# Performance work log

Hardware: AMD Instinct MI355X
Metric: run time of the kernel (lower is better)

## Reference

```python
import jax, jax.numpy as jnp
import numpy as np

NUM_EMBEDDINGS = 16384
EMBED_DIM = 256
COMMITMENT_COST = 0.25  # legacy=True: vq_loss = commit + beta * codebook


def setup_inputs() -> dict:
    key = jax.random.key(0)
    k1, k2, k3, k4 = jax.random.split(key, 4)
    z = jax.random.normal(k1, (8, 2048, EMBED_DIM), dtype=jnp.float32)
    # frozen codebook: normal(0, embedding_dim ** -0.5)
    codebook = jax.random.normal(k2, (NUM_EMBEDDINGS, EMBED_DIM), dtype=jnp.float32) * (EMBED_DIM ** -0.5)
    # learnable linear projection, torch default uniform init
    bound = 1.0 / np.sqrt(EMBED_DIM)
    proj_w = jax.random.uniform(k3, (EMBED_DIM, EMBED_DIM), dtype=jnp.float32, minval=-bound, maxval=bound)
    proj_b = jax.random.uniform(k4, (EMBED_DIM,), dtype=jnp.float32, minval=-bound, maxval=bound)
    return {"z": z, "codebook": codebook, "proj_w": proj_w, "proj_b": proj_b}


def reference(z, codebook, proj_w, proj_b):
    B, T, D = z.shape
    # projected codebook (the only learned part of the quantizer)
    quant_codebook = codebook @ proj_w.T + proj_b  # [K, D]
    z_flat = z.reshape(-1, D)  # [N, D]
    # squared L2 distances: ||z||^2 + ||c||^2 - 2 z.c
    dists = (
        jnp.sum(z_flat * z_flat, axis=1, keepdims=True)
        + jnp.sum(quant_codebook * quant_codebook, axis=1)
        - 2.0 * jnp.einsum("nd,kd->nk", z_flat, quant_codebook)
    )  # [N, K]
    idx = jnp.argmin(dists, axis=1)  # [N]
    quantized = quant_codebook[idx].reshape(z.shape)  # [B, T, D]

    commitment_loss = jnp.mean((jax.lax.stop_gradient(quantized) - z) ** 2)
    codebook_loss = jnp.mean((quantized - jax.lax.stop_gradient(z)) ** 2)
    vq_loss = commitment_loss + COMMITMENT_COST * codebook_loss  # legacy formulation

    # straight-through estimator
    quantized = z + jax.lax.stop_gradient(quantized - z)
    encoding_indices = idx.reshape(B, T)
    return quantized, vq_loss, encoding_indices
```

## Files before the change

### kernel.cpp

```cpp
#include <hip/hip_runtime.h>

typedef unsigned short u16;
typedef __bf16 bf16x8 __attribute__((ext_vector_type(8)));
typedef float f32x4 __attribute__((ext_vector_type(4)));

#define NQ 16384
#define NC 16384
#define DD 256
#define BM 256
#define BN 256
#define BK 32
#define NSPLIT 8
#define NPART (NSPLIT * 2)
#define NTILES ((NC / NSPLIT) / BN)
#define NSTEPS (NTILES * 8)

__device__ __forceinline__ u16 f2bf(float x) {
  unsigned u = __float_as_uint(x);
  u += 0x7fffu + ((u >> 16) & 1u);
  return (u16)(u >> 16);
}
__device__ __forceinline__ float bf2f(u16 h) {
  return __uint_as_float(((unsigned)h) << 16);
}

__device__ __forceinline__ void gl2lds16(const void* g, void* l) {
  __builtin_amdgcn_global_load_lds((__attribute__((address_space(1))) void*)g,
                                   (__attribute__((address_space(3))) void*)l,
                                   16, 0, 0);
}

#define MFMA_AGPR(ACC, A, B) \
  asm("v_mfma_f32_16x16x32_bf16 %0, %1, %2, %0" : "+a"(ACC) : "v"(A), "v"(B))

__global__ __launch_bounds__(256) void split_z_kernel(const float* __restrict__ z,
                                                      u16* __restrict__ Ah,
                                                      u16* __restrict__ Al) {
  size_t i = (size_t)blockIdx.x * 256 + threadIdx.x;
  float4 v = ((const float4*)z)[i];
  float f[4] = {v.x, v.y, v.z, v.w};
  u16 hh[4], ll[4];
#pragma unroll
  for (int j = 0; j < 4; ++j) {
    hh[j] = f2bf(f[j]);
    ll[j] = f2bf(f[j] - bf2f(hh[j]));
  }
  ushort4 h; h.x = hh[0]; h.y = hh[1]; h.z = hh[2]; h.w = hh[3];
  ushort4 l; l.x = ll[0]; l.y = ll[1]; l.z = ll[2]; l.w = ll[3];
  ((ushort4*)Ah)[i] = h;
  ((ushort4*)Al)[i] = l;
}

__global__ __launch_bounds__(256) void norm256_kernel(const float* __restrict__ x,
                                                      float* __restrict__ nrm) {
  const int t = threadIdx.x;
  const int j = t & 7;
  const int row = blockIdx.x * 32 + (t >> 3);
  const float* q = x + (size_t)row * 256;
  float half[2];
#pragma unroll
  for (int h = 0; h < 2; ++h) {
    const float* p = q + h * 128;
    float v0 = p[j];
    float r = __fmul_rn(v0, v0);
#pragma unroll
    for (int i = 8; i < 128; i += 8) {
      float v = p[i + j];
      r = __fadd_rn(r, __fmul_rn(v, v));
    }
    float s1 = __fadd_rn(r, __shfl_xor(r, 1));
    float s2 = __fadd_rn(s1, __shfl_xor(s1, 2));
    half[h] = __fadd_rn(s2, __shfl_xor(s2, 4));
  }
  if (j == 0) nrm[row] = __fadd_rn(half[0], half[1]);
}

__global__ __launch_bounds__(256) void qc_gemm_kernel(const float* __restrict__ cb,
                                                      const float* __restrict__ W,
                                                      const float* __restrict__ bias,
                                                      float* __restrict__ qc) {
  __shared__ float As[64][33];
  __shared__ float Bs[64][33];
  const int bm = blockIdx.x >> 2;
  const int bn = blockIdx.x & 3;
  const int m0 = bm * 64, n0 = bn * 64;
  const int t = threadIdx.x;
  const int tx = t & 15, ty = t >> 4;
  float acc[4][4] = {};
  for (int kc = 0; kc < 256; kc += 32) {
    __syncthreads();
#pragma unroll
    for (int j = 0; j < 8; ++j) {
      int idx = j * 256 + t;
      int r = idx >> 5, c = idx & 31;
      As[r][c] = cb[(size_t)(m0 + r) * 256 + kc + c];
      Bs[r][c] = W[(size_t)(n0 + r) * 256 + kc + c];
    }
    __syncthreads();
#pragma unroll
    for (int kk = 0; kk < 32; ++kk) {
      float a[4], b[4];
#pragma unroll
      for (int u = 0; u < 4; ++u) a[u] = As[ty * 4 + u][kk];
#pragma unroll
      for (int v = 0; v < 4; ++v) b[v] = Bs[tx * 4 + v][kk];
#pragma unroll
      for (int u = 0; u < 4; ++u)
#pragma unroll
        for (int v = 0; v < 4; ++v) acc[u][v] += a[u] * b[v];
    }
  }
#pragma unroll
  for (int u = 0; u < 4; ++u)
#pragma unroll
    for (int v = 0; v < 4; ++v) {
      int r = m0 + ty * 4 + u, c = n0 + tx * 4 + v;
      qc[(size_t)r * 256 + c] = acc[u][v] + bias[c];
    }
}

__global__ __launch_bounds__(256) void split_qc_kernel(const float* __restrict__ qc,
                                                       u16* __restrict__ Bh,
                                                       u16* __restrict__ Bl) {
  size_t i = (size_t)blockIdx.x * 256 + threadIdx.x;
  float4 v = ((const float4*)qc)[i];
  float f[4] = {v.x, v.y, v.z, v.w};
  u16 hh[4], ll[4];
#pragma unroll
  for (int j = 0; j < 4; ++j) {
    hh[j] = f2bf(f[j]);
    ll[j] = f2bf(f[j] - bf2f(hh[j]));
  }
  ushort4 h; h.x = hh[0]; h.y = hh[1]; h.z = hh[2]; h.w = hh[3];
  ushort4 l; l.x = ll[0]; l.y = ll[1]; l.z = ll[2]; l.w = ll[3];
  ((ushort4*)Bh)[i] = h;
  ((ushort4*)Bl)[i] = l;
}

__global__ __launch_bounds__(512, 2) void vq_argmin_kernel(
    const u16* __restrict__ Ah, const u16* __restrict__ Al,
    const u16* __restrict__ Bh, const u16* __restrict__ Bl,
    const float* __restrict__ cnorm, const float* __restrict__ znorm,
    float* __restrict__ pval, int* __restrict__ pidx) {
  __shared__ __align__(16) u16 Ahs[2][BM * BK];
  __shared__ __align__(16) u16 Als[2][BM * BK];
  __shared__ __align__(16) u16 Bhs[2][BN * BK];
  __shared__ __align__(16) u16 Bls[2][BN * BK];

  const int bm = blockIdx.x / NSPLIT;
  const int spl = blockIdx.x % NSPLIT;
  const int lane = threadIdx.x & 63;
  const int wid = threadIdx.x >> 6;
  const int wm = wid >> 1, wn = wid & 1;
  const int l15 = lane & 15;
  const int lg = lane >> 4;
  const int m0 = bm * BM;
  const int ns0 = spl * (NC / NSPLIT);

  const int st_r = lane >> 2;
  const int st_k = (((lane & 3) ^ ((lane >> 3) & 3)) << 3);

  const int rd_sw = ((lg ^ ((l15 >> 1) & 3)) << 3);

  auto stage = [&](int buf, int s) {
    const int ntt = s >> 3;
    const int kcc = (s & 7) * BK;
    const int nn0 = ns0 + ntt * BN;
#pragma unroll
    for (int j = 0; j < 2; ++j) {
      const int grp = wid * 2 + j;
      const int r = grp * 16 + st_r;
      const size_t ga = (size_t)(m0 + r) * DD + kcc + st_k;
      const size_t gb = (size_t)(nn0 + r) * DD + kcc + st_k;
      gl2lds16(Ah + ga, &Ahs[buf][grp * 512]);
      gl2lds16(Al + ga, &Als[buf][grp * 512]);
      gl2lds16(Bh + gb, &Bhs[buf][grp * 512]);
      gl2lds16(Bl + gb, &Bls[buf][grp * 512]);
    }
  };

  float rmin[4][4];
  int ridx[4][4];
#pragma unroll
  for (int a = 0; a < 4; ++a)
#pragma unroll
    for (int b = 0; b < 4; ++b) { rmin[a][b] = 3.4e38f; ridx[a][b] = 0; }

  stage(0, 0);
  asm volatile("s_waitcnt vmcnt(0)" ::: "memory");
  __builtin_amdgcn_s_barrier();

  for (int nt = 0; nt < NTILES; ++nt) {
    const int n0 = ns0 + nt * BN;
    f32x4 acc[4][8];
#pragma unroll
    for (int a = 0; a < 4; ++a)
#pragma unroll
      for (int b = 0; b < 8; ++b) {
        f32x4 zz = {0.f, 0.f, 0.f, 0.f};
        acc[a][b] = zz;
      }

#pragma unroll 1
    for (int k8 = 0; k8 < 8; ++k8) {
      const int s = nt * 8 + k8;
      const int cur = s & 1;

      __builtin_amdgcn_s_barrier();
      if (s + 1 < NSTEPS) {
        stage(cur ^ 1, s + 1);
        asm volatile("s_waitcnt vmcnt(8)" ::: "memory");
      } else {
        asm volatile("s_waitcnt vmcnt(0)" ::: "memory");
      }
      __builtin_amdgcn_s_barrier();
      __builtin_amdgcn_sched_barrier(0);

      bf16x8 ah[4], al[4];
#pragma unroll
      for (int mi = 0; mi < 4; ++mi) {
        const int r = wm * 64 + mi * 16 + l15;
        const int off = r * BK + rd_sw;
        ah[mi] = *(const bf16x8*)&Ahs[cur][off];
        al[mi] = *(const bf16x8*)&Als[cur][off];
      }
      bf16x8 bh[4][2], bl[4][2];
#pragma unroll
      for (int u = 0; u < 2; ++u) {
        const int r = wn * 128 + u * 16 + l15;
        const int off = r * BK + rd_sw;
        bh[0][u] = *(const bf16x8*)&Bhs[cur][off];
        bl[0][u] = *(const bf16x8*)&Bls[cur][off];
      }
      __builtin_amdgcn_s_setprio(1);
#pragma unroll
      for (int p = 0; p < 4; ++p) {
        if (p < 3) {
#pragma unroll
          for (int u = 0; u < 2; ++u) {
            const int r = wn * 128 + ((p + 1) * 2 + u) * 16 + l15;
            const int off = r * BK + rd_sw;
            bh[p + 1][u] = *(const bf16x8*)&Bhs[cur][off];
            bl[p + 1][u] = *(const bf16x8*)&Bls[cur][off];
          }
        }
#pragma unroll
        for (int u = 0; u < 2; ++u)
#pragma unroll
          for (int mi = 0; mi < 4; ++mi)
            MFMA_AGPR(acc[mi][p * 2 + u], ah[mi], bh[p][u]);
#pragma unroll
        for (int u = 0; u < 2; ++u)
#pragma unroll
          for (int mi = 0; mi < 4; ++mi)
            MFMA_AGPR(acc[mi][p * 2 + u], ah[mi], bl[p][u]);
#pragma unroll
        for (int u = 0; u < 2; ++u)
#pragma unroll
          for (int mi = 0; mi < 4; ++mi)
            MFMA_AGPR(acc[mi][p * 2 + u], al[mi], bh[p][u]);
        __builtin_amdgcn_sched_barrier(0);
      }
      __builtin_amdgcn_s_setprio(0);
    }

    float cnv[8];
#pragma unroll
    for (int ni = 0; ni < 8; ++ni)
      cnv[ni] = cnorm[n0 + wn * 128 + ni * 16 + l15];
#pragma unroll
    for (int mi = 0; mi < 4; ++mi) {
      float zr[4];
#pragma unroll
      for (int i = 0; i < 4; ++i)
        zr[i] = znorm[m0 + wm * 64 + mi * 16 + lg * 4 + i];
#pragma unroll
      for (int ni = 0; ni < 8; ++ni) {
        const int col = n0 + wn * 128 + ni * 16 + l15;
        const float cn = cnv[ni];
#pragma unroll
        for (int i = 0; i < 4; ++i) {
          const float s = __fadd_rn(zr[i], cn);
          const float v = __fsub_rn(s, __fmul_rn(2.0f, acc[mi][ni][i]));
          if (v < rmin[mi][i]) { rmin[mi][i] = v; ridx[mi][i] = col; }
        }
      }
    }
  }
#pragma unroll
  for (int mi = 0; mi < 4; ++mi)
#pragma unroll
    for (int i = 0; i < 4; ++i) {
      float v = rmin[mi][i];
      int ix = ridx[mi][i];
#pragma unroll
      for (int d = 1; d < 16; d <<= 1) {
        float ov = __shfl_xor(v, d);
        int oi = __shfl_xor(ix, d);
        if (ov < v || (ov == v && oi < ix)) { v = ov; ix = oi; }
      }
      if (l15 == 0) {
        const int row = m0 + wm * 64 + mi * 16 + lg * 4 + i;
        const int part = spl * 2 + wn;
        pval[(size_t)part * NQ + row] = v;
        pidx[(size_t)part * NQ + row] = ix;
      }
    }
}

__global__ __launch_bounds__(256) void finalize_kernel(
    const float* __restrict__ pval, const int* __restrict__ pidx,
    const float* __restrict__ qc, const float* __restrict__ z,
    float* __restrict__ out, float* __restrict__ loss_acc) {
  __shared__ int sidx[8];
  __shared__ float red[256];
  const int bid = blockIdx.x;
  const int t = threadIdx.x;
  if (t < 8) {
    const int row = bid * 8 + t;
    float best = pval[row];
    int bi = pidx[row];
    for (int s2 = 1; s2 < NPART; ++s2) {
      float v = pval[(size_t)s2 * NQ + row];
      int ix = pidx[(size_t)s2 * NQ + row];
      if (v < best || (v == best && ix < bi)) { best = v; bi = ix; }
    }
    sidx[t] = bi;
    out[4194305 + row] = (float)bi;
  }
  __syncthreads();
  float d2 = 0.f;
#pragma unroll
  for (int r = 0; r < 8; ++r) {
    const int row = bid * 8 + r;
    const int ix = sidx[r];
    const float q = qc[(size_t)ix * 256 + t];
    const float zz = z[(size_t)row * 256 + t];
    out[(size_t)row * 256 + t] = q;
    const float d = q - zz;
    d2 += d * d;
  }
  red[t] = d2;
  for (int st = 128; st; st >>= 1) {
    __syncthreads();
    if (t < st) red[t] += red[t + st];
  }
  if (t == 0) atomicAdd(loss_acc, red[0]);
}

__global__ void write_loss_kernel(const float* __restrict__ loss_acc, float* __restrict__ out) {
  out[4194304] = 1.25f * loss_acc[0] / 4194304.0f;
}

extern "C" void kernel_launch(void* const* d_in, const int* in_sizes, int n_in,
                              void* d_out, int out_size, void* d_ws, size_t ws_size,
                              hipStream_t stream) {
  const float* z = (const float*)d_in[0];
  const float* cb = (const float*)d_in[1];
  const float* W = (const float*)d_in[2];
  const float* bias = (const float*)d_in[3];
  float* out = (float*)d_out;
  char* ws = (char*)d_ws;

  constexpr size_t OFF_QC = 0;
  constexpr size_t OFF_AH = OFF_QC + 16777216;
  constexpr size_t OFF_AL = OFF_AH + 8388608;
  constexpr size_t OFF_BH = OFF_AL + 8388608;
  constexpr size_t OFF_BL = OFF_BH + 8388608;
  constexpr size_t OFF_CN = OFF_BL + 8388608;
  constexpr size_t OFF_ZN = OFF_CN + 65536;
  constexpr size_t OFF_PV = OFF_ZN + 65536;
  constexpr size_t OFF_PI = OFF_PV + 1048576;
  constexpr size_t OFF_ACC = OFF_PI + 1048576;

  float* qc = (float*)(ws + OFF_QC);
  u16* Ah = (u16*)(ws + OFF_AH);
  u16* Al = (u16*)(ws + OFF_AL);
  u16* Bh = (u16*)(ws + OFF_BH);
  u16* Bl = (u16*)(ws + OFF_BL);
  float* cn = (float*)(ws + OFF_CN);
  float* zn = (float*)(ws + OFF_ZN);
  float* pv = (float*)(ws + OFF_PV);
  int* pi = (int*)(ws + OFF_PI);
  float* lacc = (float*)(ws + OFF_ACC);

  hipMemsetAsync(lacc, 0, 4, stream);
  split_z_kernel<<<4096, 256, 0, stream>>>(z, Ah, Al);
  qc_gemm_kernel<<<1024, 256, 0, stream>>>(cb, W, bias, qc);
  norm256_kernel<<<NQ / 32, 256, 0, stream>>>(z, zn);
  norm256_kernel<<<NC / 32, 256, 0, stream>>>(qc, cn);
  split_qc_kernel<<<4096, 256, 0, stream>>>(qc, Bh, Bl);
  vq_argmin_kernel<<<(NQ / BM) * NSPLIT, 512, 0, stream>>>(Ah, Al, Bh, Bl, cn, zn, pv, pi);
  finalize_kernel<<<NQ / 8, 256, 0, stream>>>(pv, pi, qc, z, out, lacc);
  write_loss_kernel<<<1, 1, 0, stream>>>(lacc, out);
}
```

Measured before the change: 535.0 us.

## Split MFMA inner loop into barrier-synced phases with ping-pong B fragments

Restructures the per-K-step compute into four phases, each preceded by a workgroup barrier plus lgkmcnt(0) wait, using two ping-pong register sets for B fragments instead of a 4-deep array. Waves are forced to alternate between LDS reads and MFMA clusters in lockstep, with priority raised only during the MFMA clusters. The staging lambda also precomputes per-thread global and LDS offsets to cut address arithmetic. Extra barriers add sync cost and may serialize LDS latency instead of overlapping it.

```diff
diff --git a/kernel.cpp b/kernel.cpp
--- a/kernel.cpp
+++ b/kernel.cpp
@@ -137,6 +137,36 @@
   ((ushort4*)Bl)[i] = l;
 }
 
+
+#define READPAIR(P, BH, BL) do { \
+    { const int r_ = wn * 128 + ((P) * 2 + 0) * 16 + l15; \
+      const int o_ = r_ * BK + rd_sw; \
+      (BH)[0] = *(const bf16x8*)&Bhs[cur][o_]; \
+      (BL)[0] = *(const bf16x8*)&Bls[cur][o_]; } \
+    { const int r_ = wn * 128 + ((P) * 2 + 1) * 16 + l15; \
+      const int o_ = r_ * BK + rd_sw; \
+      (BH)[1] = *(const bf16x8*)&Bhs[cur][o_]; \
+      (BL)[1] = *(const bf16x8*)&Bls[cur][o_]; } \
+  } while (0)
+
+#define CLUSTER(PB, BH, BL) do { \
+    _Pragma("unroll") for (int u = 0; u < 2; ++u) \
+      _Pragma("unroll") for (int mi = 0; mi < 4; ++mi) \
+        MFMA_AGPR(acc[mi][(PB) + u], ah[mi], (BH)[u]); \
+    _Pragma("unroll") for (int u = 0; u < 2; ++u) \
+      _Pragma("unroll") for (int mi = 0; mi < 4; ++mi) \
+        MFMA_AGPR(acc[mi][(PB) + u], ah[mi], (BL)[u]); \
+    _Pragma("unroll") for (int u = 0; u < 2; ++u) \
+      _Pragma("unroll") for (int mi = 0; mi < 4; ++mi) \
+        MFMA_AGPR(acc[mi][(PB) + u], al[mi], (BH)[u]); \
+  } while (0)
+
+#define PHASE_SYNC() do { \
+    __builtin_amdgcn_s_barrier(); \
+    asm volatile("s_waitcnt lgkmcnt(0)" ::: "memory"); \
+    __builtin_amdgcn_sched_barrier(0); \
+  } while (0)
+
 __global__ __launch_bounds__(512, 2) void vq_argmin_kernel(
     const u16* __restrict__ Ah, const u16* __restrict__ Al,
     const u16* __restrict__ Bh, const u16* __restrict__ Bl,
@@ -162,21 +192,26 @@
 
   const int rd_sw = ((lg ^ ((l15 >> 1) & 3)) << 3);
 
-  auto stage = [&](int buf, int s) {
-    const int ntt = s >> 3;
-    const int kcc = (s & 7) * BK;
-    const int nn0 = ns0 + ntt * BN;
-#pragma unroll
-    for (int j = 0; j < 2; ++j) {
-      const int grp = wid * 2 + j;
-      const int r = grp * 16 + st_r;
-      const size_t ga = (size_t)(m0 + r) * DD + kcc + st_k;
-      const size_t gb = (size_t)(nn0 + r) * DD + kcc + st_k;
-      gl2lds16(Ah + ga, &Ahs[buf][grp * 512]);
-      gl2lds16(Al + ga, &Als[buf][grp * 512]);
-      gl2lds16(Bh + gb, &Bhs[buf][grp * 512]);
-      gl2lds16(Bl + gb, &Bls[buf][grp * 512]);
-    }
+  const int grp0 = wid * 2, grp1 = wid * 2 + 1;
+  const int stoff0 = (grp0 * 16 + st_r) * DD + st_k;
+  const int stoff1 = (grp1 * 16 + st_r) * DD + st_k;
+  const int dst0 = grp0 * 512, dst1 = grp1 * 512;
+
+  auto stage = [&](int buf, int s2) {
+    const int kcc = (s2 & 7) * BK;
+    const u16* pAh = Ah + (size_t)m0 * DD + kcc;
+    const u16* pAl = Al + (size_t)m0 * DD + kcc;
+    const size_t bb = (size_t)(ns0 + (s2 >> 3) * BN) * DD + kcc;
+    const u16* pBh = Bh + bb;
+    const u16* pBl = Bl + bb;
+    gl2lds16(pAh + stoff0, &Ahs[buf][dst0]);
+    gl2lds16(pAl + stoff0, &Als[buf][dst0]);
+    gl2lds16(pBh + stoff0, &Bhs[buf][dst0]);
+    gl2lds16(pBl + stoff0, &Bls[buf][dst0]);
+    gl2lds16(pAh + stoff1, &Ahs[buf][dst1]);
+    gl2lds16(pAl + stoff1, &Als[buf][dst1]);
+    gl2lds16(pBh + stoff1, &Bhs[buf][dst1]);
+    gl2lds16(pBl + stoff1, &Bls[buf][dst1]);
   };
 
   float rmin[4][4];
@@ -224,43 +259,30 @@
         ah[mi] = *(const bf16x8*)&Ahs[cur][off];
         al[mi] = *(const bf16x8*)&Als[cur][off];
       }
-      bf16x8 bh[4][2], bl[4][2];
-#pragma unroll
-      for (int u = 0; u < 2; ++u) {
-        const int r = wn * 128 + u * 16 + l15;
-        const int off = r * BK + rd_sw;
-        bh[0][u] = *(const bf16x8*)&Bhs[cur][off];
-        bl[0][u] = *(const bf16x8*)&Bls[cur][off];
-      }
+      bf16x8 bhA[2], blA[2], bhB[2], blB[2];
+      READPAIR(0, bhA, blA);
+
+      PHASE_SYNC();
       __builtin_amdgcn_s_setprio(1);
-#pragma unroll
-      for (int p = 0; p < 4; ++p) {
-        if (p < 3) {
-#pragma unroll
-          for (int u = 0; u < 2; ++u) {
-            const int r = wn * 128 + ((p + 1) * 2 + u) * 16 + l15;
-            const int off = r * BK + rd_sw;
-            bh[p + 1][u] = *(const bf16x8*)&Bhs[cur][off];
-            bl[p + 1][u] = *(const bf16x8*)&Bls[cur][off];
-          }
-        }
-#pragma unroll
-        for (int u = 0; u < 2; ++u)
-#pragma unroll
-          for (int mi = 0; mi < 4; ++mi)
-            MFMA_AGPR(acc[mi][p * 2 + u], ah[mi], bh[p][u]);
-#pragma unroll
-        for (int u = 0; u < 2; ++u)
-#pragma unroll
-          for (int mi = 0; mi < 4; ++mi)
-            MFMA_AGPR(acc[mi][p * 2 + u], ah[mi], bl[p][u]);
-#pragma unroll
-        for (int u = 0; u < 2; ++u)
-#pragma unroll
-          for (int mi = 0; mi < 4; ++mi)
-            MFMA_AGPR(acc[mi][p * 2 + u], al[mi], bh[p][u]);
-        __builtin_amdgcn_sched_barrier(0);
-      }
+      CLUSTER(0, bhA, blA);
+      __builtin_amdgcn_s_setprio(0);
+      READPAIR(1, bhB, blB);
+
+      PHASE_SYNC();
+      __builtin_amdgcn_s_setprio(1);
+      CLUSTER(2, bhB, blB);
+      __builtin_amdgcn_s_setprio(0);
+      READPAIR(2, bhA, blA);
+
+      PHASE_SYNC();
+      __builtin_amdgcn_s_setprio(1);
+      CLUSTER(4, bhA, blA);
+      __builtin_amdgcn_s_setprio(0);
+      READPAIR(3, bhB, blB);
+
+      PHASE_SYNC();
+      __builtin_amdgcn_s_setprio(1);
+      CLUSTER(6, bhB, blB);
       __builtin_amdgcn_s_setprio(0);
     }
 
```

New measurement: 565.4 us. +5.7%, slower.
